# Kernel optimization log

Hardware: AMD Instinct MI355X
Metric: run time of the kernel (lower is better)

The kernel has to match this reference:

```python
import jax, jax.numpy as jnp
import numpy as np

N_HEADS, N_LEVELS, N_POINTS = 8, 4, 4
D_MODEL, UNIT = 384, 128

@jax.custom_vjp
def grl(x):
    # Gradient Reversal Layer: identity forward, -grad backward (lambda_=1)
    return x

def _grl_fwd(x):
    return x, None

def _grl_bwd(res, g):
    return (-g,)

grl.defvjp(_grl_fwd, _grl_bwd)


def ms_deform_attn_core(value, spatial_shapes_np, loc, attn):
    """Multi-scale deformable attention (grid_sample bilinear, zeros padding, align_corners=False).
    value: (N, Len_in, nH, hd)   loc: (N, Lq, nH, nL, nP, 2) normalized [0,1]   attn: (N, Lq, nH, nL, nP)
    """
    N, Lq, nH, nL, nP, _ = loc.shape
    hd = value.shape[-1]
    b = jnp.arange(N).reshape(N, 1, 1, 1)
    h = jnp.arange(nH).reshape(1, 1, nH, 1)
    out = jnp.zeros((N, Lq, nH, hd), dtype=value.dtype)
    start = 0
    for l in range(nL):
        H, W = int(spatial_shapes_np[l, 0]), int(spatial_shapes_np[l, 1])
        v = value[:, start:start + H * W]  # (N, H*W, nH, hd)
        start += H * W
        # align_corners=False pixel coords
        x = loc[:, :, :, l, :, 0] * W - 0.5
        y = loc[:, :, :, l, :, 1] * H - 0.5
        x0f, y0f = jnp.floor(x), jnp.floor(y)
        lx, ly = x - x0f, y - y0f
        x0, y0 = x0f.astype(jnp.int32), y0f.astype(jnp.int32)
        def gather(xi, yi):
            valid = ((xi >= 0) & (xi < W) & (yi >= 0) & (yi < H)).astype(value.dtype)
            flat = jnp.clip(yi, 0, H - 1) * W + jnp.clip(xi, 0, W - 1)  # (N,Lq,nH,nP)
            return v[b, flat, h] * valid[..., None]  # (N,Lq,nH,nP,hd)
        s = (((1 - lx) * (1 - ly))[..., None] * gather(x0, y0)
             + (lx * (1 - ly))[..., None] * gather(x0 + 1, y0)
             + ((1 - lx) * ly)[..., None] * gather(x0, y0 + 1)
             + (lx * ly)[..., None] * gather(x0 + 1, y0 + 1))
        out = out + jnp.sum(s * attn[:, :, :, l, :, None], axis=3)
    return out.reshape(N, Lq, nH * hd)


def setup_inputs() -> dict:
    key = jax.random.key(0)
    ks = jax.random.split(key, 12)
    N, Lq = 2, 5440
    spatial = np.array([[64, 64], [32, 32], [16, 16], [8, 8]], dtype=np.int32)
    sizes = spatial[:, 0] * spatial[:, 1]
    Len_in = int(sizes.sum())  # 5440
    lsi = np.concatenate([[0], np.cumsum(sizes)[:-1]]).astype(np.int32)
    D, U, nH, nL, nP = D_MODEL, UNIT, N_HEADS, N_LEVELS, N_POINTS
    def lin(k, fin, fout):
        return jax.random.normal(k, (fin, fout), jnp.float32) / np.sqrt(fin)
    # faithful grid-init bias for sampling offsets
    thetas = np.arange(nH) * (2.0 * np.pi / nH)
    grid = np.stack([np.cos(thetas), np.sin(thetas)], -1)
    grid = grid / np.abs(grid).max(-1, keepdims=True)
    grid = np.tile(grid.reshape(nH, 1, 1, 2), (1, nL, nP, 1))
    for i in range(nP):
        grid[:, :, i, :] *= (i + 1)
    return {
        "query": jax.random.normal(ks[0], (N, Lq, D), jnp.float32),
        "reference_points": jax.random.uniform(ks[1], (N, Lq, nL, 2), jnp.float32),
        "input_flatten": jax.random.normal(ks[2], (N, Len_in, D), jnp.float32),
        "input_spatial_shapes": jnp.asarray(spatial),
        "input_level_start_index": jnp.asarray(lsi),
        "W_off": 0.01 * jax.random.normal(ks[3], (2 * U, nH * nL * nP * 2), jnp.float32),
        "b_off": jnp.asarray(grid.reshape(-1), dtype=jnp.float32),
        "W_attn": lin(ks[4], 2 * U, nH * nL * nP),
        "b_attn": jnp.zeros((nH * nL * nP,), jnp.float32),
        "W_val": lin(ks[5], 2 * U, 3 * U),
        "b_val": jnp.zeros((3 * U,), jnp.float32),
        "W_out": lin(ks[6], 3 * U, 2 * U),
        "b_out": jnp.zeros((2 * U,), jnp.float32),
        "W_attn_zd": lin(ks[7], 3 * U, nH * nL * nP),
        "b_attn_zd": jnp.zeros((nH * nL * nP,), jnp.float32),
        "W_val_zd": lin(ks[8], D, D),
        "b_val_zd": jnp.zeros((D,), jnp.float32),
        "W_out_zd": lin(ks[9], D, U),
        "b_out_zd": jnp.zeros((U,), jnp.float32),
    }


def reference(query, reference_points, input_flatten, input_spatial_shapes, input_level_start_index,
              W_off, b_off, W_attn, b_attn, W_val, b_val, W_out, b_out,
              W_attn_zd, b_attn_zd, W_val_zd, b_val_zd, W_out_zd, b_out_zd):
    N, Lq, _ = query.shape
    nH, nL, nP, U = N_HEADS, N_LEVELS, N_POINTS, UNIT
    ss = np.asarray(input_spatial_shapes)  # static level shapes
    sample_query = query[..., :2 * U]
    off = (sample_query @ W_off + b_off).reshape(N, Lq, nH, nL, nP, 2)
    # offset normalizer = [W_l, H_l] per level
    norm = jnp.asarray(np.stack([ss[:, 1], ss[:, 0]], -1), dtype=query.dtype)
    loc = reference_points[:, :, None, :, None, :] + off / norm[None, None, None, :, None, :]
    # top (content) path
    top_val = (input_flatten[..., :2 * U] @ W_val + b_val).reshape(N, -1, nH, 3 * U // nH)
    aw = jax.nn.softmax((sample_query @ W_attn + b_attn).reshape(N, Lq, nH, nL * nP), -1)
    aw = aw.reshape(N, Lq, nH, nL, nP)
    top_out = ms_deform_attn_core(top_val, ss, loc, aw) @ W_out + b_out
    # bottom (domain) path with gradient reversal on content slice
    bot_val_in = jnp.concatenate([grl(input_flatten[..., :2 * U]), input_flatten[..., 2 * U:]], -1)
    bot_val = (bot_val_in @ W_val_zd + b_val_zd).reshape(N, -1, nH, D_MODEL // nH)
    bot_query = jnp.concatenate([grl(query[..., :2 * U]), query[..., 2 * U:]], -1)
    aw_zd = jax.nn.softmax((bot_query @ W_attn_zd + b_attn_zd).reshape(N, Lq, nH, nL * nP), -1)
    aw_zd = aw_zd.reshape(N, Lq, nH, nL, nP)
    bot_out = ms_deform_attn_core(bot_val, ss, loc, aw_zd) @ W_out_zd + b_out_zd
    return jnp.concatenate([top_out, bot_out], -1)
```

## Files before the change

### kernel.cpp

```cpp
#include <hip/hip_runtime.h>
#include <hip/hip_bf16.h>
#include <math.h>

#define DM   384
#define U2   256
#define HD   48

typedef __attribute__((ext_vector_type(8))) short short8;
typedef __attribute__((ext_vector_type(4))) float floatx4;
typedef __attribute__((ext_vector_type(2))) float floatx2;

static __device__ __forceinline__ unsigned short f2bfbits(float f) {
    __hip_bfloat16 h = __float2bfloat16(f);
    return *reinterpret_cast<unsigned short*>(&h);
}
static __device__ __forceinline__ unsigned pack2(float x, float y) {
    return (unsigned)f2bfbits(x) | ((unsigned)f2bfbits(y) << 16);
}
static __device__ __forceinline__ float bflo(unsigned u) { return __uint_as_float(u << 16); }
static __device__ __forceinline__ float bfhi(unsigned u) { return __uint_as_float(u & 0xffff0000u); }

struct PrepParams {
    const float* q; const float* f;
    __hip_bfloat16 *q_bf, *f_bf;
    const float* wsrc[7]; __hip_bfloat16* wdst[7];
    int K[7], N[7], off[8];
    int nQ4, nF4, total;
};
__global__ __launch_bounds__(256) void prep_kernel(PrepParams d) {
    const int idx = blockIdx.x * 256 + threadIdx.x;
    if (idx >= d.total) return;
    if (idx < d.nQ4) {
        const int i4 = idx * 4;
        const float4 v = *(const float4*)&d.q[i4];
        uint2 pk; pk.x = pack2(v.x, v.y); pk.y = pack2(v.z, v.w);
        *(uint2*)&d.q_bf[i4] = pk;
        return;
    }
    if (idx < d.nQ4 + d.nF4) {
        const int i4 = (idx - d.nQ4) * 4;
        const float4 v = *(const float4*)&d.f[i4];
        uint2 pk; pk.x = pack2(v.x, v.y); pk.y = pack2(v.z, v.w);
        *(uint2*)&d.f_bf[i4] = pk;
        return;
    }
    const int iw = idx - d.nQ4 - d.nF4;
    int s = 0;
#pragma unroll
    for (int i = 1; i < 7; ++i) if (iw >= d.off[i]) s = i;
    const int r = iw - d.off[s];
    const int k = r / d.N[s], n = r - k * d.N[s];
    d.wdst[s][(size_t)n * d.K[s] + k] = __float2bfloat16(d.wsrc[s][r]);
}

struct Seg {
    const __hip_bfloat16* A; int lda;
    const __hip_bfloat16* Bt; int ldbt;
    const float* bias; void* C; int ldc; int K; int omode;
};
struct SegParams { Seg seg[5]; int ystart[5]; int nseg; };

__global__ __launch_bounds__(256) void gemm_seg_kernel(SegParams p) {
    __shared__ __hip_bfloat16 As[64 * 40];
    __shared__ __hip_bfloat16 Bs[64 * 40];

    const int yb = blockIdx.y;
    int s = 0;
#pragma unroll
    for (int i = 1; i < 5; ++i) if (i < p.nseg && yb >= p.ystart[i]) s = i;
    Seg sg;
    switch (s) {
        case 0: sg = p.seg[0]; break;
        case 1: sg = p.seg[1]; break;
        case 2: sg = p.seg[2]; break;
        case 3: sg = p.seg[3]; break;
        default: sg = p.seg[4]; break;
    }
    const int by = yb - p.ystart[s];

    const int t    = threadIdx.x;
    const int bm   = blockIdx.x * 64;
    const int bn   = by * 64;
    const int w    = t >> 6, lane = t & 63;
    const int wm   = (w >> 1) * 32, wn = (w & 1) * 32;
    const int quad = lane >> 4, lm = lane & 15;

    const int r0 = t >> 2, kc = (t & 3) * 8;

    const __hip_bfloat16* Ap = sg.A  + (size_t)(bm + r0) * sg.lda  + kc;
    const __hip_bfloat16* Bp = sg.Bt + (size_t)(bn + r0) * sg.ldbt + kc;

    short8 abf = *(const short8*)Ap;
    short8 bbf = *(const short8*)Bp;

    floatx4 acc[2][2] = {};

    for (int k0 = 0; k0 < sg.K; k0 += 32) {
        *(short8*)&As[r0 * 40 + kc] = abf;
        *(short8*)&Bs[r0 * 40 + kc] = bbf;
        __syncthreads();

        const int kn = k0 + 32;
        if (kn < sg.K) {
            abf = *(const short8*)(Ap + kn);
            bbf = *(const short8*)(Bp + kn);
        }

        short8 af[2], bf[2];
#pragma unroll
        for (int i = 0; i < 2; ++i)
            af[i] = *(const short8*)&As[(wm + i * 16 + lm) * 40 + quad * 8];
#pragma unroll
        for (int j = 0; j < 2; ++j)
            bf[j] = *(const short8*)&Bs[(wn + j * 16 + lm) * 40 + quad * 8];
#pragma unroll
        for (int i = 0; i < 2; ++i)
#pragma unroll
            for (int j = 0; j < 2; ++j)
                acc[i][j] = __builtin_amdgcn_mfma_f32_16x16x32_bf16(
                    af[i], bf[j], acc[i][j], 0, 0, 0);
        __syncthreads();
    }

#pragma unroll
    for (int i = 0; i < 2; ++i)
#pragma unroll
        for (int reg = 0; reg < 4; ++reg) {
            const int row = bm + wm + i * 16 + quad * 4 + reg;
#pragma unroll
            for (int j = 0; j < 2; ++j) {
                const int col = bn + wn + j * 16 + lm;
                const float v = acc[i][j][reg] + sg.bias[col];
                if (sg.omode == 0) {
                    ((float*)sg.C)[(size_t)row * sg.ldc + col] = v;
                } else if (sg.omode == 1) {
                    ((__hip_bfloat16*)sg.C)[(size_t)row * sg.ldc + col] = __float2bfloat16(v);
                } else {
                    const int h = col / 48;
                    const size_t idx = (size_t)row * 768 + h * 96 +
                                       ((sg.omode == 3) ? 48 : 0) + (col - h * 48);
                    ((__hip_bfloat16*)sg.C)[idx] = __float2bfloat16(v);
                }
            }
        }
}

#define SPP 524

__global__ __launch_bounds__(192) void sampler_kernel(
    const float* __restrict__ off_buf,
    const float* __restrict__ logit_top,
    const float* __restrict__ logit_bot,
    const float* __restrict__ ref_pts,
    const int*   __restrict__ ss,
    const int*   __restrict__ lsi,
    const __hip_bfloat16* __restrict__ vcomb,
    __hip_bfloat16* __restrict__ core_top,
    __hip_bfloat16* __restrict__ core_bot,
    int Lq, int LenIn)
{
    __shared__ float    sA[2][128];
    __shared__ unsigned sP[2][SPP];
    __shared__ float4   sRed[96][2];

    const int bid = blockIdx.x;
    const int t   = threadIdx.x;

    float gw[4];
    int   gp[4];

    if (t < 128) {
        const int e = t;
        const int l = (e >> 2) & 3;
        const float2 offv = *(const float2*)&off_buf[(size_t)bid * 256 + 2 * e];
        const float rx = ref_pts[(size_t)(bid * 4 + l) * 2 + 0];
        const float ry = ref_pts[(size_t)(bid * 4 + l) * 2 + 1];
        const int H = ss[2 * l], W = ss[2 * l + 1];
        const int start = lsi[l];

        const float x = (rx + offv.x / (float)W) * (float)W - 0.5f;
        const float y = (ry + offv.y / (float)H) * (float)H - 0.5f;
        const float x0f = floorf(x), y0f = floorf(y);
        const float lx = x - x0f, ly = y - y0f;
        const int ix0 = (int)x0f, iy0 = (int)y0f;
        const int ix1 = ix0 + 1,  iy1 = iy0 + 1;

        const float vx0 = (ix0 >= 0 && ix0 < W) ? 1.f : 0.f;
        const float vx1 = (ix1 >= 0 && ix1 < W) ? 1.f : 0.f;
        const float vy0 = (iy0 >= 0 && iy0 < H) ? 1.f : 0.f;
        const float vy1 = (iy1 >= 0 && iy1 < H) ? 1.f : 0.f;
        const int cx0 = min(max(ix0, 0), W - 1);
        const int cx1 = min(max(ix1, 0), W - 1);
        const int cy0 = min(max(iy0, 0), H - 1);
        const int cy1 = min(max(iy1, 0), H - 1);
        const int base = bid / Lq * LenIn + start;

        gp[0] = base + cy0 * W + cx0;
        gp[1] = base + cy0 * W + cx1;
        gp[2] = base + cy1 * W + cx0;
        gp[3] = base + cy1 * W + cx1;
        gw[0] = (1.f - lx) * (1.f - ly) * vx0 * vy0;
        gw[1] = lx * (1.f - ly) * vx1 * vy0;
        gw[2] = (1.f - lx) * ly * vx0 * vy1;
        gw[3] = lx * ly * vx1 * vy1;
    }

    if (t < 16) {
        const int br = t >> 3;
        const int h  = t & 7;
        const float* L = (br ? logit_bot : logit_top) + (size_t)bid * 128 + h * 16;
        float lg[16];
        *(float4*)&lg[0]  = *(const float4*)&L[0];
        *(float4*)&lg[4]  = *(const float4*)&L[4];
        *(float4*)&lg[8]  = *(const float4*)&L[8];
        *(float4*)&lg[12] = *(const float4*)&L[12];
        float m = -1e30f;
#pragma unroll
        for (int j = 0; j < 16; ++j) m = fmaxf(m, lg[j]);
        float ex[16], sum = 0.f;
#pragma unroll
        for (int j = 0; j < 16; ++j) { ex[j] = expf(lg[j] - m); sum += ex[j]; }
        const float inv = 1.f / sum;
#pragma unroll
        for (int j = 0; j < 16; ++j) sA[br][h * 16 + j] = ex[j] * inv;
    }
    __syncthreads();

    if (t < 128) {
        const int e = t;
        const int pidx = 4 * e + (e >> 4);
#pragma unroll
        for (int br = 0; br < 2; ++br) {
            const float a = sA[br][e];
#pragma unroll
            for (int k = 0; k < 4; ++k) {
                sP[br][pidx + k] =
                    ((unsigned)f2bfbits(gw[k] * a) << 16) | (unsigned)gp[k];
            }
        }
    }
    __syncthreads();

    const int half = t / 96;
    const int u    = t - half * 96;
    const int g    = u / 6;
    const int m    = u - g * 6;
    const int br   = g & 1;
    const int h    = g >> 1;

    const unsigned* P = sP[br];
    const char* vbase = (const char*)vcomb;
    const unsigned tco = (unsigned)(h * 192 + br * 96 + m * 16);

    floatx2 ac0 = {0.f, 0.f}, ac1 = {0.f, 0.f};
    floatx2 ac2 = {0.f, 0.f}, ac3 = {0.f, 0.f};
    const int lp0 = half * 8;
#pragma unroll
    for (int lp = 0; lp < 8; ++lp) {
        const int ib = 65 * h + 4 * (lp0 + lp);
#pragma unroll
        for (int k = 0; k < 4; ++k) {
            const unsigned uu = P[ib + k];
            const float wv = __uint_as_float(uu & 0xffff0000u);
            const unsigned off = (uu & 0x3fffu) * 1536u + tco;
            const uint4 v = *(const uint4*)(vbase + off);
            floatx2 wv2 = {wv, wv};
            floatx2 f0 = {bflo(v.x), bfhi(v.x)};
            floatx2 f1 = {bflo(v.y), bfhi(v.y)};
            floatx2 f2 = {bflo(v.z), bfhi(v.z)};
            floatx2 f3 = {bflo(v.w), bfhi(v.w)};
            ac0 += wv2 * f0;
            ac1 += wv2 * f1;
            ac2 += wv2 * f2;
            ac3 += wv2 * f3;
        }
    }

    if (half) {
        float4 p0; p0.x = ac0.x; p0.y = ac0.y; p0.z = ac1.x; p0.w = ac1.y;
        float4 p1; p1.x = ac2.x; p1.y = ac2.y; p1.z = ac3.x; p1.w = ac3.y;
        sRed[u][0] = p0;
        sRed[u][1] = p1;
    }
    __syncthreads();
    if (!half) {
        const float4 p0 = sRed[u][0];
        const float4 p1 = sRed[u][1];
        uint4 o;
        o.x = pack2(ac0.x + p0.x, ac0.y + p0.y);
        o.y = pack2(ac1.x + p0.z, ac1.y + p0.w);
        o.z = pack2(ac2.x + p1.x, ac2.y + p1.y);
        o.w = pack2(ac3.x + p1.z, ac3.y + p1.w);
        __hip_bfloat16* dst = br ? core_bot : core_top;
        *(uint4*)&dst[(size_t)bid * DM + h * HD + m * 8] = o;
    }
}

extern "C" void kernel_launch(void* const* d_in, const int* in_sizes, int n_in,
                              void* d_out, int out_size, void* d_ws, size_t ws_size,
                              hipStream_t stream) {
    const float* query   = (const float*)d_in[0];
    const float* refpts  = (const float*)d_in[1];
    const float* flat    = (const float*)d_in[2];
    const int*   ss      = (const int*)d_in[3];
    const int*   lsi     = (const int*)d_in[4];
    const float* W_off   = (const float*)d_in[5];
    const float* b_off   = (const float*)d_in[6];
    const float* W_attn  = (const float*)d_in[7];
    const float* b_attn  = (const float*)d_in[8];
    const float* W_val   = (const float*)d_in[9];
    const float* b_val   = (const float*)d_in[10];
    const float* W_out   = (const float*)d_in[11];
    const float* b_out   = (const float*)d_in[12];
    const float* W_attn_zd = (const float*)d_in[13];
    const float* b_attn_zd = (const float*)d_in[14];
    const float* W_val_zd  = (const float*)d_in[15];
    const float* b_val_zd  = (const float*)d_in[16];
    const float* W_out_zd  = (const float*)d_in[17];
    const float* b_out_zd  = (const float*)d_in[18];

    const int Lq    = in_sizes[0] / (2 * DM);
    const int LenIn = in_sizes[2] / (2 * DM);
    const int M  = 2 * Lq;
    const int Mv = 2 * LenIn;

    float* out = (float*)d_out;

    float* ws      = (float*)d_ws;
    float* off_buf = ws;
    float* lt      = off_buf + (size_t)M * 256;
    float* lb      = lt + (size_t)M * 128;
    __hip_bfloat16* q_bf  = (__hip_bfloat16*)(lb + (size_t)M * 128);
    __hip_bfloat16* f_bf  = q_bf + (size_t)M * 384;
    __hip_bfloat16* vcomb = f_bf + (size_t)Mv * 384;
    __hip_bfloat16* ct    = vcomb + (size_t)Mv * 768;
    __hip_bfloat16* cb    = ct + (size_t)M * 384;
    __hip_bfloat16* wtb   = cb + (size_t)M * 384;

    PrepParams pp;
    pp.q = query; pp.f = flat;
    pp.q_bf = q_bf; pp.f_bf = f_bf;
    const float* srcs[7] = {W_attn, W_attn_zd, W_val, W_val_zd, W_out, W_out_zd, W_off};
    const int Ks[7] = {256, 384, 256, 384, 384, 384, 256};
    const int Ns[7] = {128, 128, 384, 384, 256, 128, 256};
    __hip_bfloat16* dsts[7];
    int off = 0;
    for (int i = 0; i < 7; ++i) {
        pp.wsrc[i] = srcs[i]; pp.K[i] = Ks[i]; pp.N[i] = Ns[i];
        pp.off[i] = off;
        dsts[i] = wtb + off;
        pp.wdst[i] = dsts[i];
        off += Ks[i] * Ns[i];
    }
    pp.off[7] = off;
    pp.nQ4 = M * DM / 4;
    pp.nF4 = Mv * DM / 4;
    pp.total = pp.nQ4 + pp.nF4 + off;

    const dim3 blk(256);
    const int mg = M / 64;

    prep_kernel<<<dim3((pp.total + 255) / 256), blk, 0, stream>>>(pp);

    {
        SegParams p;
        p.seg[0] = { q_bf, DM, dsts[6], 256, b_off,     off_buf, 256, 256, 0 };
        p.seg[1] = { q_bf, DM, dsts[0], 256, b_attn,    lt,      128, 256, 0 };
        p.seg[2] = { q_bf, DM, dsts[1], 384, b_attn_zd, lb,      128, 384, 0 };
        p.seg[3] = { f_bf, DM, dsts[2], 256, b_val,     vcomb,   0,   256, 2 };
        p.seg[4] = { f_bf, DM, dsts[3], 384, b_val_zd,  vcomb,   0,   384, 3 };
        p.ystart[0] = 0; p.ystart[1] = 4; p.ystart[2] = 6;
        p.ystart[3] = 8; p.ystart[4] = 14;
        p.nseg = 5;
        gemm_seg_kernel<<<dim3(mg, 20), blk, 0, stream>>>(p);
    }

    sampler_kernel<<<dim3(M), dim3(192), 0, stream>>>(
        off_buf, lt, lb, refpts, ss, lsi, vcomb, ct, cb, Lq, LenIn);

    {
        SegParams p;
        p.seg[0] = { ct, DM, dsts[4], 384, b_out,    out,      DM, 384, 0 };
        p.seg[1] = { cb, DM, dsts[5], 384, b_out_zd, out + U2, DM, 384, 0 };
        p.ystart[0] = 0; p.ystart[1] = 4;
        p.nseg = 2;
        gemm_seg_kernel<<<dim3(mg, 6), blk, 0, stream>>>(p);
    }
}
```

Baseline: 223.0 us.

## Retile segmented GEMM to 128x64 with direct global-to-LDS loads and XOR swizzle

Rewrites the segmented projection GEMM to use 128x64 output tiles with K-step 64. Tiles are loaded with global_load_lds straight into shared memory, and an XOR swizzle on the chunk index avoids LDS bank conflicts. Each wave now computes 32x64 with more MFMAs per barrier, which should improve operand reuse and cut register staging. The cost is that register prefetch double-buffering is dropped in favour of a full vmcnt wait each iteration, and the grid has half as many M blocks. M must be divisible by 128 (Lq=5440*2=10880 = 85*128) and K divisible by 64.

```diff
diff --git a/kernel.cpp b/kernel.cpp
--- a/kernel.cpp
+++ b/kernel.cpp
@@ -19,6 +19,12 @@
 }
 static __device__ __forceinline__ float bflo(unsigned u) { return __uint_as_float(u << 16); }
 static __device__ __forceinline__ float bfhi(unsigned u) { return __uint_as_float(u & 0xffff0000u); }
+
+typedef __attribute__((address_space(1))) const unsigned int guint;
+typedef __attribute__((address_space(3))) unsigned int luint;
+static __device__ __forceinline__ void gld16(const void* g, void* l) {
+    __builtin_amdgcn_global_load_lds((guint*)g, (luint*)l, 16, 0, 0);
+}
 
 struct PrepParams {
     const float* q; const float* f;
@@ -61,8 +67,8 @@
 struct SegParams { Seg seg[5]; int ystart[5]; int nseg; };
 
 __global__ __launch_bounds__(256) void gemm_seg_kernel(SegParams p) {
-    __shared__ __hip_bfloat16 As[64 * 40];
-    __shared__ __hip_bfloat16 Bs[64 * 40];
+    __shared__ __align__(16) __hip_bfloat16 As[128 * 64];
+    __shared__ __align__(16) __hip_bfloat16 Bs[64 * 64];
 
     const int yb = blockIdx.y;
     int s = 0;
@@ -79,46 +85,56 @@
     const int by = yb - p.ystart[s];
 
     const int t    = threadIdx.x;
-    const int bm   = blockIdx.x * 64;
+    const int bm   = blockIdx.x * 128;
     const int bn   = by * 64;
     const int w    = t >> 6, lane = t & 63;
-    const int wm   = (w >> 1) * 32, wn = (w & 1) * 32;
+    const int wm   = w * 32;
     const int quad = lane >> 4, lm = lane & 15;
 
-    const int r0 = t >> 2, kc = (t & 3) * 8;
-
-    const __hip_bfloat16* Ap = sg.A  + (size_t)(bm + r0) * sg.lda  + kc;
-    const __hip_bfloat16* Bp = sg.Bt + (size_t)(bn + r0) * sg.ldbt + kc;
-
-    short8 abf = *(const short8*)Ap;
-    short8 bbf = *(const short8*)Bp;
-
-    floatx4 acc[2][2] = {};
-
-    for (int k0 = 0; k0 < sg.K; k0 += 32) {
-        *(short8*)&As[r0 * 40 + kc] = abf;
-        *(short8*)&Bs[r0 * 40 + kc] = bbf;
+    floatx4 acc[2][4] = {};
+
+    for (int k0 = 0; k0 < sg.K; k0 += 64) {
+#pragma unroll
+        for (int j = 0; j < 4; ++j) {
+            const int u = j * 256 + t;
+            const int r = u >> 3, c = u & 7;
+            gld16(sg.A + (size_t)(bm + r) * sg.lda + k0 + ((c ^ (r & 7)) << 3),
+                  &As[j * 2048 + w * 512]);
+        }
+#pragma unroll
+        for (int j = 0; j < 2; ++j) {
+            const int u = j * 256 + t;
+            const int r = u >> 3, c = u & 7;
+            gld16(sg.Bt + (size_t)(bn + r) * sg.ldbt + k0 + ((c ^ (r & 7)) << 3),
+                  &Bs[j * 2048 + w * 512]);
+        }
+        asm volatile("s_waitcnt vmcnt(0)" ::: "memory");
         __syncthreads();
 
-        const int kn = k0 + 32;
-        if (kn < sg.K) {
-            abf = *(const short8*)(Ap + kn);
-            bbf = *(const short8*)(Bp + kn);
-        }
-
-        short8 af[2], bf[2];
-#pragma unroll
-        for (int i = 0; i < 2; ++i)
-            af[i] = *(const short8*)&As[(wm + i * 16 + lm) * 40 + quad * 8];
-#pragma unroll
-        for (int j = 0; j < 2; ++j)
-            bf[j] = *(const short8*)&Bs[(wn + j * 16 + lm) * 40 + quad * 8];
-#pragma unroll
-        for (int i = 0; i < 2; ++i)
-#pragma unroll
-            for (int j = 0; j < 2; ++j)
-                acc[i][j] = __builtin_amdgcn_mfma_f32_16x16x32_bf16(
-                    af[i], bf[j], acc[i][j], 0, 0, 0);
+        short8 af[2][2], bfr[2][4];
+#pragma unroll
+        for (int kk = 0; kk < 2; ++kk) {
+#pragma unroll
+            for (int i = 0; i < 2; ++i) {
+                const int row = wm + i * 16 + lm;
+                const int ch  = (kk * 4 + quad) ^ (row & 7);
+                af[kk][i] = *(const short8*)&As[row * 64 + ch * 8];
+            }
+#pragma unroll
+            for (int j = 0; j < 4; ++j) {
+                const int row = j * 16 + lm;
+                const int ch  = (kk * 4 + quad) ^ (row & 7);
+                bfr[kk][j] = *(const short8*)&Bs[row * 64 + ch * 8];
+            }
+        }
+#pragma unroll
+        for (int kk = 0; kk < 2; ++kk)
+#pragma unroll
+            for (int i = 0; i < 2; ++i)
+#pragma unroll
+                for (int j = 0; j < 4; ++j)
+                    acc[i][j] = __builtin_amdgcn_mfma_f32_16x16x32_bf16(
+                        af[kk][i], bfr[kk][j], acc[i][j], 0, 0, 0);
         __syncthreads();
     }
 
@@ -128,8 +144,8 @@
         for (int reg = 0; reg < 4; ++reg) {
             const int row = bm + wm + i * 16 + quad * 4 + reg;
 #pragma unroll
-            for (int j = 0; j < 2; ++j) {
-                const int col = bn + wn + j * 16 + lm;
+            for (int j = 0; j < 4; ++j) {
+                const int col = bn + j * 16 + lm;
                 const float v = acc[i][j][reg] + sg.bias[col];
                 if (sg.omode == 0) {
                     ((float*)sg.C)[(size_t)row * sg.ldc + col] = v;
@@ -358,7 +374,7 @@
     pp.total = pp.nQ4 + pp.nF4 + off;
 
     const dim3 blk(256);
-    const int mg = M / 64;
+    const int mg = M / 128;
 
     prep_kernel<<<dim3((pp.total + 255) / 256), blk, 0, stream>>>(pp);
 
```

Result: no change. 227.0 us (+1.8%).

## Interleave batch blocks, parallelize softmax with shuffles, batch gathers, keep fp32 weights

Applied to the files above, without the earlier changes.

Remaps block IDs so consecutive blocks alternate between batch elements. The 16-thread serial softmax becomes a 64-thread one that uses the idle warps and wave shuffles for max and sum. Sample entries become uint2 so each weight stays fp32 instead of being truncated to bf16. The four gathers per level/point are issued before any FMAs to raise memory-level parallelism. This costs double the LDS for sample entries and more live registers.

```diff
diff --git a/kernel.cpp b/kernel.cpp
--- a/kernel.cpp
+++ b/kernel.cpp
@@ -159,11 +159,12 @@
     __hip_bfloat16* __restrict__ core_bot,
     int Lq, int LenIn)
 {
-    __shared__ float    sA[2][128];
-    __shared__ unsigned sP[2][SPP];
-    __shared__ float4   sRed[96][2];
-
-    const int bid = blockIdx.x;
+    __shared__ float sA[2][128];
+    __shared__ uint2 sP[2][SPP];
+    __shared__ float4 sRed[96][2];
+
+    const int bx  = blockIdx.x;
+    const int bid = (bx & 1) * Lq + (bx >> 1);
     const int t   = threadIdx.x;
 
     float gw[4];
@@ -203,26 +204,25 @@
         gw[1] = lx * (1.f - ly) * vx1 * vy0;
         gw[2] = (1.f - lx) * ly * vx0 * vy1;
         gw[3] = lx * ly * vx1 * vy1;
-    }
-
-    if (t < 16) {
-        const int br = t >> 3;
-        const int h  = t & 7;
-        const float* L = (br ? logit_bot : logit_top) + (size_t)bid * 128 + h * 16;
-        float lg[16];
-        *(float4*)&lg[0]  = *(const float4*)&L[0];
-        *(float4*)&lg[4]  = *(const float4*)&L[4];
-        *(float4*)&lg[8]  = *(const float4*)&L[8];
-        *(float4*)&lg[12] = *(const float4*)&L[12];
-        float m = -1e30f;
-#pragma unroll
-        for (int j = 0; j < 16; ++j) m = fmaxf(m, lg[j]);
-        float ex[16], sum = 0.f;
-#pragma unroll
-        for (int j = 0; j < 16; ++j) { ex[j] = expf(lg[j] - m); sum += ex[j]; }
+    } else {
+        const int lt64 = t - 128;
+        const int grp  = lt64 >> 2;
+        const int j4   = lt64 & 3;
+        const int br   = grp >> 3;
+        const int h    = grp & 7;
+        const float* L = (br ? logit_bot : logit_top) + (size_t)bid * 128 + h * 16 + j4 * 4;
+        const float4 lg = *(const float4*)L;
+        float m = fmaxf(fmaxf(lg.x, lg.y), fmaxf(lg.z, lg.w));
+        m = fmaxf(m, __shfl_xor(m, 1));
+        m = fmaxf(m, __shfl_xor(m, 2));
+        float e0 = expf(lg.x - m), e1 = expf(lg.y - m);
+        float e2 = expf(lg.z - m), e3 = expf(lg.w - m);
+        float sum = e0 + e1 + e2 + e3;
+        sum += __shfl_xor(sum, 1);
+        sum += __shfl_xor(sum, 2);
         const float inv = 1.f / sum;
-#pragma unroll
-        for (int j = 0; j < 16; ++j) sA[br][h * 16 + j] = ex[j] * inv;
+        float* dst = &sA[br][h * 16 + j4 * 4];
+        dst[0] = e0 * inv; dst[1] = e1 * inv; dst[2] = e2 * inv; dst[3] = e3 * inv;
     }
     __syncthreads();
 
@@ -234,8 +234,10 @@
             const float a = sA[br][e];
 #pragma unroll
             for (int k = 0; k < 4; ++k) {
-                sP[br][pidx + k] =
-                    ((unsigned)f2bfbits(gw[k] * a) << 16) | (unsigned)gp[k];
+                uint2 pr;
+                pr.x = (unsigned)gp[k];
+                pr.y = __float_as_uint(gw[k] * a);
+                sP[br][pidx + k] = pr;
             }
         }
     }
@@ -248,7 +250,7 @@
     const int br   = g & 1;
     const int h    = g >> 1;
 
-    const unsigned* P = sP[br];
+    const uint2* P = sP[br];
     const char* vbase = (const char*)vcomb;
     const unsigned tco = (unsigned)(h * 192 + br * 96 + m * 16);
 
@@ -258,17 +260,21 @@
 #pragma unroll
     for (int lp = 0; lp < 8; ++lp) {
         const int ib = 65 * h + 4 * (lp0 + lp);
+        uint2 pr[4];
+#pragma unroll
+        for (int k = 0; k < 4; ++k) pr[k] = P[ib + k];
+        uint4 v[4];
+#pragma unroll
+        for (int k = 0; k < 4; ++k)
+            v[k] = *(const uint4*)(vbase + ((pr[k].x & 0x3fffu) * 1536u + tco));
 #pragma unroll
         for (int k = 0; k < 4; ++k) {
-            const unsigned uu = P[ib + k];
-            const float wv = __uint_as_float(uu & 0xffff0000u);
-            const unsigned off = (uu & 0x3fffu) * 1536u + tco;
-            const uint4 v = *(const uint4*)(vbase + off);
+            const float wv = __uint_as_float(pr[k].y);
             floatx2 wv2 = {wv, wv};
-            floatx2 f0 = {bflo(v.x), bfhi(v.x)};
-            floatx2 f1 = {bflo(v.y), bfhi(v.y)};
-            floatx2 f2 = {bflo(v.z), bfhi(v.z)};
-            floatx2 f3 = {bflo(v.w), bfhi(v.w)};
+            floatx2 f0 = {bflo(v[k].x), bfhi(v[k].x)};
+            floatx2 f1 = {bflo(v[k].y), bfhi(v[k].y)};
+            floatx2 f2 = {bflo(v[k].z), bfhi(v[k].z)};
+            floatx2 f3 = {bflo(v[k].w), bfhi(v[k].w)};
             ac0 += wv2 * f0;
             ac1 += wv2 * f1;
             ac2 += wv2 * f2;
```

Result: no change. 221.7 us (-0.6%).
